# Optimization experiments

Measured on AMD Instinct MI355X. Metric: run time of the kernel, lower is better.

The kernel has to match this reference:

```python
import jax, jax.numpy as jnp
import numpy as np


def conv2d(x, w, b, pad=0, groups=1):
    y = jax.lax.conv_general_dilated(
        x, w, (1, 1), [(pad, pad), (pad, pad)],
        dimension_numbers=('NCHW', 'OIHW', 'NCHW'), feature_group_count=groups)
    return y + b[None, :, None, None]


def layernorm(x, w, b, eps=1e-5):
    # per-pixel LayerNorm over channel dim (matches to_3d -> nn.LayerNorm(dim) -> to_4d)
    mu = x.mean(1, keepdims=True)
    var = ((x - mu) ** 2).mean(1, keepdims=True)
    return (x - mu) * jax.lax.rsqrt(var + eps) * w[None, :, None, None] + b[None, :, None, None]


def setup_inputs():
    key = jax.random.key(0)
    ks = jax.random.split(key, 16)
    B, C, H, W = 1, 64, 64, 64
    heads, dh = 8, 8
    inner = heads * dh          # 64
    hid_lc = 32                 # max(16, inner // 2)
    hid_f = 4 * C               # 256, ffn_expansion_factor = 4
    def s(k, shape, fan):
        return (jax.random.normal(k, shape, jnp.float32) / np.float32(np.sqrt(fan)))
    return {
        'x': jax.random.normal(ks[0], (B, C, H, W), jnp.float32),
        'luma': jax.random.uniform(ks[1], (B, 1, H, W), jnp.float32),
        'ln1_w': jnp.ones((C,), jnp.float32), 'ln1_b': jnp.zeros((C,), jnp.float32),
        'qkv_w': s(ks[2], (3 * inner, C, 1, 1), C), 'qkv_b': jnp.zeros((3 * inner,), jnp.float32),
        'proj_w': s(ks[3], (C, inner, 1, 1), inner), 'proj_b': jnp.zeros((C,), jnp.float32),
        'lc1_w': s(ks[4], (hid_lc, 1, 3, 3), 9), 'lc1_b': jnp.zeros((hid_lc,), jnp.float32),
        'lc2_w': s(ks[5], (hid_lc, hid_lc, 3, 3), 9 * hid_lc), 'lc2_b': jnp.zeros((hid_lc,), jnp.float32),
        'gam_w': s(ks[6], (inner, hid_lc, 1, 1), hid_lc), 'gam_b': jnp.zeros((inner,), jnp.float32),
        'bet_w': s(ks[7], (inner, hid_lc, 1, 1), hid_lc), 'bet_b': jnp.zeros((inner,), jnp.float32),
        'alpha': jnp.float32(0.1),
        'ln2_w': jnp.ones((C,), jnp.float32), 'ln2_b': jnp.zeros((C,), jnp.float32),
        'ffn1_w': s(ks[8], (hid_f, C, 1, 1), C), 'ffn1_b': jnp.zeros((hid_f,), jnp.float32),
        'dw_w': s(ks[9], (hid_f, 1, 3, 3), 9), 'dw_b': jnp.zeros((hid_f,), jnp.float32),
        'ffn2_w': s(ks[10], (C, hid_f, 1, 1), hid_f), 'ffn2_b': jnp.zeros((C,), jnp.float32),
    }


def reference(x, luma, ln1_w, ln1_b, qkv_w, qkv_b, proj_w, proj_b,
              lc1_w, lc1_b, lc2_w, lc2_b, gam_w, gam_b, bet_w, bet_b, alpha,
              ln2_w, ln2_b, ffn1_w, ffn1_b, dw_w, dw_b, ffn2_w, ffn2_b):
    B, C, H, W = x.shape
    heads = 8
    N = H * W
    # --- attention branch ---
    xn = layernorm(x, ln1_w, ln1_b)
    qkv = conv2d(xn, qkv_w, qkv_b)             # [B, 3*inner, H, W]
    inner = qkv.shape[1] // 3
    dh = inner // heads

    def to_bhnd(t):  # b (h d) x y -> b h (x y) d
        return t.reshape(B, heads, dh, N).transpose(0, 1, 3, 2)

    q, k, v = [to_bhnd(t) for t in jnp.split(qkv, 3, axis=1)]
    # luma conditioning
    h1 = jax.nn.relu(conv2d(luma, lc1_w, lc1_b, pad=1))
    h1 = jax.nn.relu(conv2d(h1, lc2_w, lc2_b, pad=1))
    g = to_bhnd(conv2d(h1, gam_w, gam_b))
    bt = to_bhnd(conv2d(h1, bet_w, bet_b))
    q = g * q + bt
    k = g * k + bt
    v = g * v + bt
    # additive luma bias on q (avg_pool2d 3x3, count_include_pad=True -> fixed /9)
    invL = 1.0 - luma
    invL = jax.lax.reduce_window(invL, 0.0, jax.lax.add, (1, 1, 3, 3), (1, 1, 1, 1),
                                 [(0, 0), (0, 0), (1, 1), (1, 1)]) / 9.0
    invL = invL.reshape(B, N)
    invL = invL - invL.mean(-1, keepdims=True)
    q = q + alpha * invL[:, None, :, None]
    scale = dh ** -0.5
    attn = jax.nn.softmax(jnp.einsum('bhid,bhjd->bhij', q, k) * scale, axis=-1)
    out = jnp.einsum('bhij,bhjd->bhid', attn, v)
    out = out.transpose(0, 1, 3, 2).reshape(B, inner, H, W)
    x = x + conv2d(out, proj_w, proj_b)
    # --- ConvFFN branch ---
    y = layernorm(x, ln2_w, ln2_b)
    y = conv2d(y, ffn1_w, ffn1_b)
    y = conv2d(y, dw_w, dw_b, pad=1, groups=y.shape[1])
    y = jax.nn.gelu(y, approximate=False)
    y = conv2d(y, ffn2_w, ffn2_b)
    return x + y
```

## Files before the change

### kernel.cpp

```cpp
#include <hip/hip_runtime.h>
#include <math.h>

#define NPIX 4096
#define IMG 64
#define NBLK 512

typedef __attribute__((ext_vector_type(8))) short bf16x8;
typedef __attribute__((ext_vector_type(4))) float floatx4;
typedef __attribute__((ext_vector_type(4))) unsigned int uintx4;

__device__ __forceinline__ unsigned int split_pack(float x) {
  unsigned int u = __float_as_uint(x);
  unsigned int hif = u & 0xffff0000u;
  float lof = x - __uint_as_float(hif);
  return (u >> 16) | (__float_as_uint(lof) & 0xffff0000u);
}

__device__ __forceinline__ unsigned int pack_hi2(float a, float b) {
  return __builtin_amdgcn_perm(__float_as_uint(b), __float_as_uint(a),
                               0x07060302u);
}

__device__ __forceinline__ void stA_f32(float* p, float v) {
  __hip_atomic_store(p, v, __ATOMIC_RELAXED, __HIP_MEMORY_SCOPE_AGENT);
}
__device__ __forceinline__ void stA_u32(void* p, unsigned int v) {
  __hip_atomic_store((unsigned int*)p, v, __ATOMIC_RELAXED,
                     __HIP_MEMORY_SCOPE_AGENT);
}
__device__ __forceinline__ void stA_u64(void* p, unsigned long long v) {
  __hip_atomic_store((unsigned long long*)p, v, __ATOMIC_RELAXED,
                     __HIP_MEMORY_SCOPE_AGENT);
}
__device__ __forceinline__ unsigned int ldA(const unsigned int* p) {
  return __hip_atomic_load(p, __ATOMIC_RELAXED, __HIP_MEMORY_SCOPE_AGENT);
}
__device__ __forceinline__ unsigned int addA(unsigned int* p) {
  return __hip_atomic_fetch_add(p, 1u, __ATOMIC_RELAXED,
                                __HIP_MEMORY_SCOPE_AGENT);
}

__device__ __forceinline__ void gbar(unsigned int* base, int bid) {
  __syncthreads();
  if (threadIdx.x == 0) {
    int g = bid >> 6;
    unsigned int* ga = base + g * 32;
    unsigned int old = addA(ga);
    if (old == 63u) {
      addA(base + 256);
      while (ldA(base + 256) < 8u) __builtin_amdgcn_s_sleep(1);
      stA_u32(ga + 16, 1u);
    } else {
      while (ldA(ga + 16) == 0u) __builtin_amdgcn_s_sleep(2);
    }
    asm volatile("" ::: "memory");
  }
  __syncthreads();
}

struct S1 {
  float lum[144];
  float sw1[288];
  float tin[32][100];
  float swt[4][32][9];
  float red[64];
};
struct S2 {
  float xs[64][32];
  float wsh[64][64];
  float h2s[32][32];
  float wgs[32][64];
  float wbs[32][64];
  float mu[32];
  float rs[32];
};
struct S4 {
  float at[64][34];
  float wsh[64][64];
  float xsl[64][34];
  float ps[16][32];
  float pq[16][32];
  float mus[32];
  float rss[32];
};
struct S5 {
  float xs2[16][260];
  float wshT[32][260];
};
union SU {
  S1 s1;
  S2 s2;
  S4 s4;
  S5 s5;
};

__global__ void init_kernel(unsigned int* __restrict__ ctr,
                            unsigned short* __restrict__ cbuf) {
  int t = threadIdx.x;
#pragma unroll
  for (int i = 0; i < 8; i++) ctr[t + i * 256] = 0u;
  if (t < 16) cbuf[t] = (t < 8) ? 0x3F80 : 0;
}

__global__ __launch_bounds__(256, 3) void fused_kernel(
    const float* __restrict__ x, const float* __restrict__ luma,
    const float* __restrict__ lc1w, const float* __restrict__ lc1b,
    const float* __restrict__ lc2w, const float* __restrict__ lc2b,
    const float* __restrict__ ln1w, const float* __restrict__ ln1b,
    const float* __restrict__ qkvW, const float* __restrict__ qkvB,
    const float* __restrict__ gamW, const float* __restrict__ gamB,
    const float* __restrict__ betW, const float* __restrict__ betB,
    const float* __restrict__ alpha, const float* __restrict__ projW,
    const float* __restrict__ projB, const float* __restrict__ ln2w,
    const float* __restrict__ ln2b, const float* __restrict__ ffn1W,
    const float* __restrict__ ffn1B, const float* __restrict__ dww,
    const float* __restrict__ dwb, const float* __restrict__ ffn2W,
    const float* __restrict__ ffn2B, float* __restrict__ out,
    float* __restrict__ pooled, float* __restrict__ bsums,
    unsigned short* __restrict__ cbuf, float* __restrict__ mu1,
    float* __restrict__ rs1, unsigned short* __restrict__ qhl,
    unsigned short* __restrict__ khl, unsigned short* __restrict__ vthx,
    unsigned short* __restrict__ vtlx, float* __restrict__ pacc,
    float* __restrict__ pl, float* __restrict__ x1, float* __restrict__ f1,
    float* __restrict__ h2, unsigned int* __restrict__ ctr) {
  __shared__ SU u;
  int bid = blockIdx.x;
  int tid = threadIdx.x;

  {
    int tile = bid >> 3, ocg = bid & 7;
    int ty0 = (tile >> 3) * 8, tx0 = (tile & 7) * 8;
    float(&lum)[144] = u.s1.lum;
    float(&sw1)[288] = u.s1.sw1;
    float(&tin)[32][100] = u.s1.tin;
    float(&swt)[4][32][9] = u.s1.swt;
    float(&red)[64] = u.s1.red;
    if (tid < 144) {
      int py = tid / 12, px = tid - py * 12;
      int gy = ty0 + py - 2, gx = tx0 + px - 2;
      lum[tid] = (gy >= 0 && gy < IMG && gx >= 0 && gx < IMG)
                     ? luma[gy * IMG + gx]
                     : 0.f;
    }
    for (int idx = tid; idx < 288; idx += 256) sw1[idx] = lc1w[idx];
    for (int idx = tid; idx < 1152; idx += 256) {
      int o = idx / 288, r = idx - o * 288;
      swt[o][r / 9][r % 9] = lc2w[(ocg * 4 + o) * 288 + r];
    }
    __syncthreads();
    for (int idx = tid; idx < 3200; idx += 256) {
      int ic = idx / 100, pos = idx - ic * 100;
      int py = pos / 10, px = pos - py * 10;
      int gy = ty0 + py - 1, gx = tx0 + px - 1;
      float v = 0.f;
      if (gy >= 0 && gy < IMG && gx >= 0 && gx < IMG) {
        float s = lc1b[ic];
        const float* wp = &sw1[ic * 9];
#pragma unroll
        for (int dy = 0; dy < 3; dy++)
#pragma unroll
          for (int dx = 0; dx < 3; dx++)
            s = fmaf(wp[dy * 3 + dx], lum[(py + dy) * 12 + px + dx], s);
        v = fmaxf(s, 0.f);
      }
      tin[ic][pos] = v;
    }
    __syncthreads();
    int o = tid >> 6, pix = tid & 63;
    int ly = pix >> 3, lx = pix & 7;
    int p = (ty0 + ly) * IMG + tx0 + lx;
    float acc = lc2b[ocg * 4 + o];
    for (int ic = 0; ic < 32; ic++) {
      float v[9];
#pragma unroll
      for (int dy = 0; dy < 3; dy++)
#pragma unroll
        for (int dx = 0; dx < 3; dx++)
          v[dy * 3 + dx] = tin[ic][(ly + dy) * 10 + lx + dx];
#pragma unroll
      for (int t = 0; t < 9; t++) acc = fmaf(swt[o][ic][t], v[t], acc);
    }
    stA_f32(&h2[(ocg * 4 + o) * NPIX + p], fmaxf(acc, 0.f));
    if (ocg == 0) {
      if (tid < 64) {
        int gy = ty0 + ly, gx = tx0 + lx;
        float sv = 0.f;
#pragma unroll
        for (int dy = 0; dy < 3; dy++)
#pragma unroll
          for (int dx = 0; dx < 3; dx++)
            sv += lum[(ly + dy + 1) * 12 + lx + dx + 1];
        float cy = 3.f - (gy == 0 ? 1.f : 0.f) - (gy == 63 ? 1.f : 0.f);
        float cx = 3.f - (gx == 0 ? 1.f : 0.f) - (gx == 63 ? 1.f : 0.f);
        float pv = (cy * cx - sv) * (1.f / 9.f);
        stA_f32(&pooled[p], pv);
        red[tid] = pv;
      }
      __syncthreads();
      for (int st = 32; st > 0; st >>= 1) {
        if (tid < st) red[tid] += red[tid + st];
        __syncthreads();
      }
      if (tid == 0) stA_f32(&bsums[tile], red[0]);
      if (tid < 64) {
        float s = 0.f, q = 0.f;
#pragma unroll 8
        for (int cc = 0; cc < 64; cc++) {
          float xv = x[cc * NPIX + p];
          s += xv;
          q = fmaf(xv, xv, q);
        }
        float mu = s * (1.f / 64.f);
        stA_f32(&mu1[p], mu);
        stA_f32(&rs1[p], rsqrtf(q * (1.f / 64.f) - mu * mu + 1e-5f));
      }
    }
  }
  gbar(ctr + 0, bid);

  {
    const float QSCALE = 0.35355339059327376f * 1.4426950408889634f;
    float(&xs)[64][32] = u.s2.xs;
    float(&wsh)[64][64] = u.s2.wsh;
    float(&h2s)[32][32] = u.s2.h2s;
    float(&wgs)[32][64] = u.s2.wgs;
    float(&wbs)[32][64] = u.s2.wbs;
    float(&mu)[32] = u.s2.mu;
    float(&rs)[32] = u.s2.rs;
    int n0 = (bid & 127) * 32, part = bid >> 7;
    int m0 = (part < 2 ? part : 2) * 64;
    if (tid < 32) {
      mu[tid] = mu1[n0 + tid];
      rs[tid] = rs1[n0 + tid];
    }
    {
      int e = tid * 2;
      int c = e >> 3, off = (e & 7) * 4;
      *(float4*)&xs[c][off] = *(const float4*)&x[c * NPIX + n0 + off];
      int e1 = e + 1;
      int c1 = e1 >> 3, off1 = (e1 & 7) * 4;
      *(float4*)&xs[c1][off1] = *(const float4*)&x[c1 * NPIX + n0 + off1];
    }
    {
      int m = tid >> 2, kg = (tid & 3) * 16;
      const float4* wr = (const float4*)&qkvW[(m0 + m) * 64 + kg];
      float4 w0 = wr[0], w1 = wr[1], w2 = wr[2], w3 = wr[3];
      float wv[16] = {w0.x, w0.y, w0.z, w0.w, w1.x, w1.y, w1.z, w1.w,
                      w2.x, w2.y, w2.z, w2.w, w3.x, w3.y, w3.z, w3.w};
#pragma unroll
      for (int j = 0; j < 16; j++) wsh[kg + j][m] = wv[j];
    }
    {
      int k = tid >> 3, nf = (tid & 7) * 4;
      *(float4*)&h2s[k][nf] = *(const float4*)&h2[k * NPIX + n0 + nf];
    }
    {
      int m = tid >> 2, kg = (tid & 3) * 8;
      const float4* g0 = (const float4*)&gamW[m * 32 + kg];
      float4 a = g0[0], b4 = g0[1];
      float gv[8] = {a.x, a.y, a.z, a.w, b4.x, b4.y, b4.z, b4.w};
#pragma unroll
      for (int j = 0; j < 8; j++) wgs[kg + j][m] = gv[j];
      const float4* bb0 = (const float4*)&betW[m * 32 + kg];
      float4 c4 = bb0[0], d4 = bb0[1];
      float bv[8] = {c4.x, c4.y, c4.z, c4.w, d4.x, d4.y, d4.z, d4.w};
#pragma unroll
      for (int j = 0; j < 8; j++) wbs[kg + j][m] = bv[j];
    }
    __syncthreads();
    {
      int c = tid >> 2, pg = (tid & 3) * 8;
      float wc = ln1w[c], bc = ln1b[c];
#pragma unroll
      for (int j = 0; j < 8; j++) {
        int p = pg + j;
        xs[c][p] = (xs[c][p] - mu[p]) * rs[p] * wc + bc;
      }
    }
    __syncthreads();
    int tx = tid & 15, ty = tid >> 4;
    float ga[4][2] = {}, ba[4][2] = {};
#pragma unroll 8
    for (int kk = 0; kk < 32; kk++) {
      float4 wg4 = *(const float4*)&wgs[kk][ty * 4];
      float4 wb4 = *(const float4*)&wbs[kk][ty * 4];
      float2 h22 = *(const float2*)&h2s[kk][tx * 2];
      float gv[4] = {wg4.x, wg4.y, wg4.z, wg4.w};
      float bv[4] = {wb4.x, wb4.y, wb4.z, wb4.w};
      float hv[2] = {h22.x, h22.y};
#pragma unroll
      for (int im = 0; im < 4; im++)
#pragma unroll
        for (int in = 0; in < 2; in++) {
          ga[im][in] = fmaf(gv[im], hv[in], ga[im][in]);
          ba[im][in] = fmaf(bv[im], hv[in], ba[im][in]);
        }
    }
#pragma unroll
    for (int im = 0; im < 4; im++) {
      int cc = ty * 4 + im;
      float gb = gamB[cc], bb2 = betB[cc];
#pragma unroll
      for (int in = 0; in < 2; in++) {
        ga[im][in] += gb;
        ba[im][in] += bb2;
      }
    }
    float acc[4][2] = {};
#pragma unroll 8
    for (int kk = 0; kk < 64; kk++) {
      float4 a = *(const float4*)&wsh[kk][ty * 4];
      float2 b2 = *(const float2*)&xs[kk][tx * 2];
      float av[4] = {a.x, a.y, a.z, a.w};
      float bv[2] = {b2.x, b2.y};
#pragma unroll
      for (int im = 0; im < 4; im++)
#pragma unroll
        for (int in = 0; in < 2; in++)
          acc[im][in] = fmaf(av[im], bv[in], acc[im][in]);
    }
    float val[4][2];
#pragma unroll
    for (int im = 0; im < 4; im++) {
      int cc = ty * 4 + im;
      float bv = qkvB[m0 + cc];
#pragma unroll
      for (int in = 0; in < 2; in++)
        val[im][in] = fmaf(ga[im][in], acc[im][in] + bv, ba[im][in]);
    }
    if (part == 0) {
      float msum = 0.f;
      for (int t = 0; t < 64; t++) msum += bsums[t];
      float mean = msum * (1.f / 4096.f);
      float a0 = alpha[0];
      const float2 pv = *(const float2*)&pooled[n0 + tx * 2];
      float iv[2] = {a0 * (pv.x - mean), a0 * (pv.y - mean)};
#pragma unroll
      for (int im = 0; im < 4; im++)
#pragma unroll
        for (int in = 0; in < 2; in++)
          val[im][in] = (val[im][in] + iv[in]) * QSCALE;
    }
    if (part < 2) {
      unsigned short* dst = (part == 0) ? qhl : khl;
      int hh = ty >> 1, d0 = (ty & 1) * 4;
#pragma unroll
      for (int in = 0; in < 2; in++) {
        int n = n0 + tx * 2 + in;
        unsigned int pk[4];
#pragma unroll
        for (int im = 0; im < 4; im++) pk[im] = split_pack(val[im][in]);
        short4 hi, lo;
        hi.x = (short)(pk[0] & 0xffffu); hi.y = (short)(pk[1] & 0xffffu);
        hi.z = (short)(pk[2] & 0xffffu); hi.w = (short)(pk[3] & 0xffffu);
        lo.x = (short)(pk[0] >> 16); lo.y = (short)(pk[1] >> 16);
        lo.z = (short)(pk[2] >> 16); lo.w = (short)(pk[3] >> 16);
        unsigned short* base = dst + ((size_t)(hh * NPIX + n) << 4) + d0;
        stA_u64(base, __builtin_bit_cast(unsigned long long, hi));
        stA_u64(base + 8, __builtin_bit_cast(unsigned long long, lo));
      }
    } else {
      int nq = n0 + tx * 2;
      int off0 = (nq >> 5) * 32 + ((nq >> 4) & 1) * 4 + ((nq >> 2) & 3) * 8 +
                 (nq & 3);
#pragma unroll
      for (int im = 0; im < 4; im++) {
        int cc = ty * 4 + im;
        unsigned int pk0 = split_pack(val[im][0]);
        unsigned int pk1 = split_pack(val[im][1]);
        if (part == 2) {
          short2 hi;
          hi.x = (short)(pk0 & 0xffffu);
          hi.y = (short)(pk1 & 0xffffu);
          stA_u32(vthx + (size_t)cc * NPIX + off0,
                  __builtin_bit_cast(unsigned int, hi));
        } else {
          short2 lo;
          lo.x = (short)(pk0 >> 16);
          lo.y = (short)(pk1 >> 16);
          stA_u32(vtlx + (size_t)cc * NPIX + off0,
                  __builtin_bit_cast(unsigned int, lo));
        }
      }
    }
  }
  gbar(ctr + 512, bid);

  {
    int wave = tid >> 6, lane = tid & 63;
    int g = lane >> 4, c = lane & 15;
#pragma unroll 1
    for (int rep = 0; rep < 2; rep++) {
      int unit = bid * 2 + rep;
      int h = (unit >> 4) & 7, jp = unit >> 7;
      int i0 = (unit & 15) * 256 + wave * 64;
      int jbase = jp * 512;
      bf16x8 qB[4];
#pragma unroll
      for (int t = 0; t < 4; t++)
        qB[t] = *(const bf16x8*)(qhl +
                                 ((size_t)(h * NPIX + i0 + t * 16 + c) << 4) +
                                 ((g & 1) << 3));
      const unsigned short* kp =
          khl + ((size_t)(h * NPIX + jbase + c) << 4) + ((g >> 1) << 3);
      const unsigned short* vhp;
      const unsigned short* vlp;
      int vstep;
      if (c < 8) {
        vhp = vthx + (size_t)(h * 8 + c) * NPIX + jbase + (g << 3);
        vlp = vtlx + (size_t)(h * 8 + c) * NPIX + jbase + (g << 3);
        vstep = 32;
      } else {
        vhp = (c == 8) ? cbuf : (cbuf + 8);
        vlp = cbuf + 8;
        vstep = 0;
      }
      floatx4 zero4 = {0.f, 0.f, 0.f, 0.f};
      floatx4 aH[4], aM[4];
#pragma unroll
      for (int t = 0; t < 4; t++) {
        aH[t] = zero4;
        aM[t] = zero4;
      }
#pragma unroll 4
      for (int jt = 0; jt < 16; ++jt) {
        bf16x8 ka0 = *(const bf16x8*)kp;
        bf16x8 ka1 = *(const bf16x8*)(kp + 256);
        bf16x8 avh = *(const bf16x8*)vhp;
        bf16x8 avl = *(const bf16x8*)vlp;
        kp += 512;
        vhp += vstep;
        vlp += vstep;
#pragma unroll
        for (int t = 0; t < 4; t++) {
          floatx4 s0 = __builtin_amdgcn_mfma_f32_16x16x32_bf16(ka0, qB[t],
                                                               zero4, 0, 0, 0);
          floatx4 s1 = __builtin_amdgcn_mfma_f32_16x16x32_bf16(ka1, qB[t],
                                                               zero4, 0, 0, 0);
          float p0 = __builtin_amdgcn_exp2f(fminf(s0[0], 80.f));
          float p1 = __builtin_amdgcn_exp2f(fminf(s0[1], 80.f));
          float p2 = __builtin_amdgcn_exp2f(fminf(s0[2], 80.f));
          float p3 = __builtin_amdgcn_exp2f(fminf(s0[3], 80.f));
          float p4 = __builtin_amdgcn_exp2f(fminf(s1[0], 80.f));
          float p5 = __builtin_amdgcn_exp2f(fminf(s1[1], 80.f));
          float p6 = __builtin_amdgcn_exp2f(fminf(s1[2], 80.f));
          float p7 = __builtin_amdgcn_exp2f(fminf(s1[3], 80.f));
          uintx4 bh;
          bh.x = pack_hi2(p0, p1);
          bh.y = pack_hi2(p2, p3);
          bh.z = pack_hi2(p4, p5);
          bh.w = pack_hi2(p6, p7);
          bf16x8 pbh = __builtin_bit_cast(bf16x8, bh);
          aH[t] =
              __builtin_amdgcn_mfma_f32_16x16x32_bf16(avh, pbh, aH[t], 0, 0, 0);
          aM[t] =
              __builtin_amdgcn_mfma_f32_16x16x32_bf16(avl, pbh, aM[t], 0, 0, 0);
        }
      }
#pragma unroll
      for (int t = 0; t < 4; t++) {
        floatx4 o = aH[t] + aM[t];
        if (g < 2) {
          size_t b0 = (size_t)((jp * 8 + h) * NPIX + i0 + t * 16 + c);
          float2 lo2 = make_float2(o[0], o[1]);
          float2 hi2 = make_float2(o[2], o[3]);
          stA_u64(&pacc[b0 * 8 + g * 4],
                  __builtin_bit_cast(unsigned long long, lo2));
          stA_u64(&pacc[b0 * 8 + g * 4 + 2],
                  __builtin_bit_cast(unsigned long long, hi2));
        } else if (g == 2) {
          stA_f32(&pl[(size_t)((jp * 8 + h) * NPIX + i0 + t * 16 + c)], o[0]);
        }
      }
    }
  }
  gbar(ctr + 1024, bid);

  {
    float(&at)[64][34] = u.s4.at;
    float(&wsh)[64][64] = u.s4.wsh;
    float(&xsl)[64][34] = u.s4.xsl;
    float(&ps)[16][32] = u.s4.ps;
    float(&pq)[16][32] = u.s4.pq;
    float(&mus)[32] = u.s4.mus;
    float(&rss)[32] = u.s4.rss;
    int n0 = (bid & 127) * 32;
    int ch = bid >> 7;
    int mm = tid >> 2, kg = (tid & 3) * 16;
    {
      const float4* wr = (const float4*)&projW[mm * 64 + kg];
      float4 w0 = wr[0], w1 = wr[1], w2 = wr[2], w3 = wr[3];
      float wv[16] = {w0.x, w0.y, w0.z, w0.w, w1.x, w1.y, w1.z, w1.w,
                      w2.x, w2.y, w2.z, w2.w, w3.x, w3.y, w3.z, w3.w};
#pragma unroll
      for (int j = 0; j < 16; j++) wsh[kg + j][mm] = wv[j];
    }
    {
      int hh = tid >> 5, nn = tid & 31;
      int i = n0 + nn;
      float L = 0.f, o[8] = {};
#pragma unroll
      for (int p = 0; p < 8; p++) {
        size_t base = (size_t)((p * 8 + hh) * NPIX + i);
        L += pl[base];
        const float4 a0 = *(const float4*)&pacc[base * 8];
        const float4 a1 = *(const float4*)&pacc[base * 8 + 4];
        o[0] += a0.x; o[1] += a0.y; o[2] += a0.z; o[3] += a0.w;
        o[4] += a1.x; o[5] += a1.y; o[6] += a1.z; o[7] += a1.w;
      }
      float inv = 1.f / L;
#pragma unroll
      for (int d = 0; d < 8; d++) at[hh * 8 + d][nn] = o[d] * inv;
    }
    __syncthreads();
    int mq = tid >> 4, pp = (tid & 15) * 2;
    float acc[4][2] = {};
#pragma unroll 8
    for (int k = 0; k < 64; k++) {
      float4 w4 = *(const float4*)&wsh[k][mq * 4];
      float2 b2 = *(const float2*)&at[k][pp];
      acc[0][0] = fmaf(w4.x, b2.x, acc[0][0]);
      acc[0][1] = fmaf(w4.x, b2.y, acc[0][1]);
      acc[1][0] = fmaf(w4.y, b2.x, acc[1][0]);
      acc[1][1] = fmaf(w4.y, b2.y, acc[1][1]);
      acc[2][0] = fmaf(w4.z, b2.x, acc[2][0]);
      acc[2][1] = fmaf(w4.z, b2.y, acc[2][1]);
      acc[3][0] = fmaf(w4.w, b2.x, acc[3][0]);
      acc[3][1] = fmaf(w4.w, b2.y, acc[3][1]);
    }
    float v[4][2], sn0 = 0.f, sn1 = 0.f, qn0 = 0.f, qn1 = 0.f;
#pragma unroll
    for (int im = 0; im < 4; im++) {
      int row = mq * 4 + im;
      float bpv = projB[row];
      const float2 xr = *(const float2*)&x[row * NPIX + n0 + pp];
      float v0 = acc[im][0] + bpv + xr.x;
      float v1 = acc[im][1] + bpv + xr.y;
      v[im][0] = v0;
      v[im][1] = v1;
      sn0 += v0;
      qn0 = fmaf(v0, v0, qn0);
      sn1 += v1;
      qn1 = fmaf(v1, v1, qn1);
    }
    if (ch == 0) {
#pragma unroll
      for (int im = 0; im < 4; im++)
        stA_u64(&x1[(mq * 4 + im) * NPIX + n0 + pp],
                __builtin_bit_cast(unsigned long long,
                                   make_float2(v[im][0], v[im][1])));
    }
    ps[mq][pp] = sn0;
    ps[mq][pp + 1] = sn1;
    pq[mq][pp] = qn0;
    pq[mq][pp + 1] = qn1;
    __syncthreads();
    {
      const float4* w1r = (const float4*)&ffn1W[(ch * 64 + mm) * 64 + kg];
      float4 u0 = w1r[0], u1 = w1r[1], u2 = w1r[2], u3 = w1r[3];
      float uv[16] = {u0.x, u0.y, u0.z, u0.w, u1.x, u1.y, u1.z, u1.w,
                      u2.x, u2.y, u2.z, u2.w, u3.x, u3.y, u3.z, u3.w};
#pragma unroll
      for (int j = 0; j < 16; j++) wsh[kg + j][mm] = uv[j];
    }
    if (tid < 32) {
      float s = 0.f, q = 0.f;
#pragma unroll
      for (int t = 0; t < 16; t++) {
        s += ps[t][tid];
        q += pq[t][tid];
      }
      float mu = s * (1.f / 64.f);
      mus[tid] = mu;
      rss[tid] = rsqrtf(q * (1.f / 64.f) - mu * mu + 1e-5f);
    }
    __syncthreads();
    {
      float mu0 = mus[pp], mu1v = mus[pp + 1];
      float rs0 = rss[pp], rs1v = rss[pp + 1];
#pragma unroll
      for (int im = 0; im < 4; im++) {
        int row = mq * 4 + im;
        float w2v = ln2w[row], b2v = ln2b[row];
        *(float2*)&xsl[row][pp] =
            make_float2((v[im][0] - mu0) * rs0 * w2v + b2v,
                        (v[im][1] - mu1v) * rs1v * w2v + b2v);
      }
    }
    __syncthreads();
    float a2[4][2] = {};
#pragma unroll 8
    for (int k = 0; k < 64; k++) {
      float4 w4 = *(const float4*)&wsh[k][mq * 4];
      float2 b2 = *(const float2*)&xsl[k][pp];
      a2[0][0] = fmaf(w4.x, b2.x, a2[0][0]);
      a2[0][1] = fmaf(w4.x, b2.y, a2[0][1]);
      a2[1][0] = fmaf(w4.y, b2.x, a2[1][0]);
      a2[1][1] = fmaf(w4.y, b2.y, a2[1][1]);
      a2[2][0] = fmaf(w4.z, b2.x, a2[2][0]);
      a2[2][1] = fmaf(w4.z, b2.y, a2[2][1]);
      a2[3][0] = fmaf(w4.w, b2.x, a2[3][0]);
      a2[3][1] = fmaf(w4.w, b2.y, a2[3][1]);
    }
#pragma unroll
    for (int im = 0; im < 4; im++) {
      int row = ch * 64 + mq * 4 + im;
      float bb = ffn1B[row];
      stA_u64(&f1[row * NPIX + n0 + pp],
              __builtin_bit_cast(unsigned long long,
                                 make_float2(a2[im][0] + bb, a2[im][1] + bb)));
    }
  }
  gbar(ctr + 1536, bid);

  {
    float(&xs2)[16][260] = u.s5.xs2;
    float(&wshT)[32][260] = u.s5.wshT;
    int n0 = (bid & 255) * 16, m0 = (bid >> 8) * 32;
    int y = n0 >> 6, x0 = n0 & 63;
    {
      int mm = tid >> 3, kg = (tid & 7) * 32;
      const float4* src = (const float4*)&ffn2W[(m0 + mm) * 256 + kg];
      float4* dst = (float4*)&wshT[mm][kg];
#pragma unroll
      for (int i = 0; i < 8; i++) dst[i] = src[i];
    }
    {
      int px4 = (tid & 3) * 4;
      int xabs = x0 + px4;
#pragma unroll
      for (int k = 0; k < 4; k++) {
        int c = (tid >> 2) + 64 * k;
        const float* base = f1 + c * NPIX;
        float wv[9];
#pragma unroll
        for (int i = 0; i < 9; i++) wv[i] = dww[c * 9 + i];
        float bc = dwb[c];
        float a[4] = {bc, bc, bc, bc};
#pragma unroll
        for (int dy = 0; dy < 3; dy++) {
          int yy = y + dy - 1;
          if (yy < 0 || yy > 63) continue;
          const float* row = base + yy * IMG + xabs;
          float4 mid = *(const float4*)row;
          float left = (xabs > 0) ? row[-1] : 0.f;
          float right = (xabs + 4 < IMG) ? row[4] : 0.f;
          float win[6] = {left, mid.x, mid.y, mid.z, mid.w, right};
#pragma unroll
          for (int o = 0; o < 4; o++)
#pragma unroll
            for (int dx = 0; dx < 3; dx++)
              a[o] = fmaf(wv[dy * 3 + dx], win[o + dx], a[o]);
        }
#pragma unroll
        for (int o = 0; o < 4; o++)
          xs2[px4 + o][c] =
              0.5f * a[o] * (1.f + erff(a[o] * 0.70710678118654752f));
      }
    }
    __syncthreads();
    int m = tid >> 3, np = (tid & 7) * 2;
    float a0 = 0.f, a1 = 0.f;
#pragma unroll 4
    for (int k4 = 0; k4 < 64; k4++) {
      float4 w4 = *(const float4*)&wshT[m][k4 * 4];
      float4 xa = *(const float4*)&xs2[np][k4 * 4];
      float4 xb = *(const float4*)&xs2[np + 1][k4 * 4];
      a0 = fmaf(w4.x, xa.x, a0);
      a1 = fmaf(w4.x, xb.x, a1);
      a0 = fmaf(w4.y, xa.y, a0);
      a1 = fmaf(w4.y, xb.y, a1);
      a0 = fmaf(w4.z, xa.z, a0);
      a1 = fmaf(w4.z, xb.z, a1);
      a0 = fmaf(w4.w, xa.w, a0);
      a1 = fmaf(w4.w, xb.w, a1);
    }
    int row = m0 + m;
    float bv = ffn2B[row];
    const float2 rr = *(const float2*)&x1[row * NPIX + n0 + np];
    *(float2*)&out[row * NPIX + n0 + np] =
        make_float2(a0 + bv + rr.x, a1 + bv + rr.y);
  }
}

extern "C" void kernel_launch(void* const* d_in, const int* in_sizes, int n_in,
                              void* d_out, int out_size, void* d_ws,
                              size_t ws_size, hipStream_t stream) {
  const float* x      = (const float*)d_in[0];
  const float* luma   = (const float*)d_in[1];
  const float* ln1_w  = (const float*)d_in[2];
  const float* ln1_b  = (const float*)d_in[3];
  const float* qkv_w  = (const float*)d_in[4];
  const float* qkv_b  = (const float*)d_in[5];
  const float* proj_w = (const float*)d_in[6];
  const float* proj_b = (const float*)d_in[7];
  const float* lc1_w  = (const float*)d_in[8];
  const float* lc1_b  = (const float*)d_in[9];
  const float* lc2_w  = (const float*)d_in[10];
  const float* lc2_b  = (const float*)d_in[11];
  const float* gam_w  = (const float*)d_in[12];
  const float* gam_b  = (const float*)d_in[13];
  const float* bet_w  = (const float*)d_in[14];
  const float* bet_b  = (const float*)d_in[15];
  const float* alpha  = (const float*)d_in[16];
  const float* ln2_w  = (const float*)d_in[17];
  const float* ln2_b  = (const float*)d_in[18];
  const float* ffn1_w = (const float*)d_in[19];
  const float* ffn1_b = (const float*)d_in[20];
  const float* dw_w   = (const float*)d_in[21];
  const float* dw_b   = (const float*)d_in[22];
  const float* ffn2_w = (const float*)d_in[23];
  const float* ffn2_b = (const float*)d_in[24];
  float* out = (float*)d_out;

  float* w = (float*)d_ws;
  float* pooled = w + 0;
  float* bsums  = w + 4096;
  unsigned short* cbuf = (unsigned short*)(w + 4160);
  float* mu1 = w + 4224;
  float* rs1 = w + 8320;
  unsigned short* qhl  = (unsigned short*)(w + 12416);
  unsigned short* khl  = (unsigned short*)(w + 274560);
  unsigned short* vthx = (unsigned short*)(w + 536704);
  unsigned short* vtlx = (unsigned short*)(w + 667776);
  float* pacc = w + 798848;
  float* pl   = w + 2896000;
  float* x1   = w + 3158144;
  float* f1   = w + 3420288;
  float* h2   = w + 4468864;
  unsigned int* ctr = (unsigned int*)(w + 4599936);

  init_kernel<<<1, 256, 0, stream>>>(ctr, cbuf);
  fused_kernel<<<dim3(NBLK), 256, 0, stream>>>(
      x, luma, lc1_w, lc1_b, lc2_w, lc2_b, ln1_w, ln1_b, qkv_w, qkv_b, gam_w,
      gam_b, bet_w, bet_b, alpha, proj_w, proj_b, ln2_w, ln2_b, ffn1_w, ffn1_b,
      dw_w, dw_b, ffn2_w, ffn2_b, out, pooled, bsums, cbuf, mu1, rs1, qhl, khl,
      vthx, vtlx, pacc, pl, x1, f1, h2, ctr);
}
```

Before: 208.9 us.

## Recompute LN1 stats locally and halve attention key splits per block

LayerNorm-1 mean and rstd are now computed in stage 2 from the x tile already in shared memory, using a two-level reduction. This removes the phase-1 per-pixel pass over x and the global mu1/rs1 round trip. The attention stage also changes from two work units per block over 512 keys each to one unit per block over 1024 keys, so there are 4 key partitions instead of 8. The projection stage therefore sums 4 partial accumulators instead of 8. This cuts partial-sum traffic and reduction work, at the cost of a longer serial key loop per block and some redundant stats work across the three qkv parts.

```diff
diff --git a/kernel.cpp b/kernel.cpp
--- a/kernel.cpp
+++ b/kernel.cpp
@@ -71,6 +71,8 @@
   float h2s[32][32];
   float wgs[32][64];
   float wbs[32][64];
+  float pss[8][32];
+  float pqq[8][32];
   float mu[32];
   float rs[32];
 };
@@ -117,8 +119,7 @@
     const float* __restrict__ dwb, const float* __restrict__ ffn2W,
     const float* __restrict__ ffn2B, float* __restrict__ out,
     float* __restrict__ pooled, float* __restrict__ bsums,
-    unsigned short* __restrict__ cbuf, float* __restrict__ mu1,
-    float* __restrict__ rs1, unsigned short* __restrict__ qhl,
+    unsigned short* __restrict__ cbuf, unsigned short* __restrict__ qhl,
     unsigned short* __restrict__ khl, unsigned short* __restrict__ vthx,
     unsigned short* __restrict__ vtlx, float* __restrict__ pacc,
     float* __restrict__ pl, float* __restrict__ x1, float* __restrict__ f1,
@@ -202,18 +203,6 @@
         __syncthreads();
       }
       if (tid == 0) stA_f32(&bsums[tile], red[0]);
-      if (tid < 64) {
-        float s = 0.f, q = 0.f;
-#pragma unroll 8
-        for (int cc = 0; cc < 64; cc++) {
-          float xv = x[cc * NPIX + p];
-          s += xv;
-          q = fmaf(xv, xv, q);
-        }
-        float mu = s * (1.f / 64.f);
-        stA_f32(&mu1[p], mu);
-        stA_f32(&rs1[p], rsqrtf(q * (1.f / 64.f) - mu * mu + 1e-5f));
-      }
     }
   }
   gbar(ctr + 0, bid);
@@ -225,14 +214,12 @@
     float(&h2s)[32][32] = u.s2.h2s;
     float(&wgs)[32][64] = u.s2.wgs;
     float(&wbs)[32][64] = u.s2.wbs;
+    float(&pss)[8][32] = u.s2.pss;
+    float(&pqq)[8][32] = u.s2.pqq;
     float(&mu)[32] = u.s2.mu;
     float(&rs)[32] = u.s2.rs;
     int n0 = (bid & 127) * 32, part = bid >> 7;
     int m0 = (part < 2 ? part : 2) * 64;
-    if (tid < 32) {
-      mu[tid] = mu1[n0 + tid];
-      rs[tid] = rs1[n0 + tid];
-    }
     {
       int e = tid * 2;
       int c = e >> 3, off = (e & 7) * 4;
@@ -266,6 +253,31 @@
       float bv[8] = {c4.x, c4.y, c4.z, c4.w, d4.x, d4.y, d4.z, d4.w};
 #pragma unroll
       for (int j = 0; j < 8; j++) wbs[kg + j][m] = bv[j];
+    }
+    __syncthreads();
+    {
+      int p = tid & 31, i = tid >> 5;
+      float s = 0.f, q = 0.f;
+#pragma unroll
+      for (int j = 0; j < 8; j++) {
+        float xv = xs[i * 8 + j][p];
+        s += xv;
+        q = fmaf(xv, xv, q);
+      }
+      pss[i][p] = s;
+      pqq[i][p] = q;
+    }
+    __syncthreads();
+    if (tid < 32) {
+      float s = 0.f, q = 0.f;
+#pragma unroll
+      for (int i = 0; i < 8; i++) {
+        s += pss[i][tid];
+        q += pqq[i][tid];
+      }
+      float m = s * (1.f / 64.f);
+      mu[tid] = m;
+      rs[tid] = rsqrtf(q * (1.f / 64.f) - m * m + 1e-5f);
     }
     __syncthreads();
     {
@@ -389,88 +401,84 @@
   {
     int wave = tid >> 6, lane = tid & 63;
     int g = lane >> 4, c = lane & 15;
-#pragma unroll 1
-    for (int rep = 0; rep < 2; rep++) {
-      int unit = bid * 2 + rep;
-      int h = (unit >> 4) & 7, jp = unit >> 7;
-      int i0 = (unit & 15) * 256 + wave * 64;
-      int jbase = jp * 512;
-      bf16x8 qB[4];
-#pragma unroll
-      for (int t = 0; t < 4; t++)
-        qB[t] = *(const bf16x8*)(qhl +
-                                 ((size_t)(h * NPIX + i0 + t * 16 + c) << 4) +
-                                 ((g & 1) << 3));
-      const unsigned short* kp =
-          khl + ((size_t)(h * NPIX + jbase + c) << 4) + ((g >> 1) << 3);
-      const unsigned short* vhp;
-      const unsigned short* vlp;
-      int vstep;
-      if (c < 8) {
-        vhp = vthx + (size_t)(h * 8 + c) * NPIX + jbase + (g << 3);
-        vlp = vtlx + (size_t)(h * 8 + c) * NPIX + jbase + (g << 3);
-        vstep = 32;
-      } else {
-        vhp = (c == 8) ? cbuf : (cbuf + 8);
-        vlp = cbuf + 8;
-        vstep = 0;
-      }
-      floatx4 zero4 = {0.f, 0.f, 0.f, 0.f};
-      floatx4 aH[4], aM[4];
+    int h = (bid >> 4) & 7, jp = bid >> 7;
+    int i0 = (bid & 15) * 256 + wave * 64;
+    int jbase = jp * 1024;
+    bf16x8 qB[4];
+#pragma unroll
+    for (int t = 0; t < 4; t++)
+      qB[t] = *(const bf16x8*)(qhl +
+                               ((size_t)(h * NPIX + i0 + t * 16 + c) << 4) +
+                               ((g & 1) << 3));
+    const unsigned short* kp =
+        khl + ((size_t)(h * NPIX + jbase + c) << 4) + ((g >> 1) << 3);
+    const unsigned short* vhp;
+    const unsigned short* vlp;
+    int vstep;
+    if (c < 8) {
+      vhp = vthx + (size_t)(h * 8 + c) * NPIX + jbase + (g << 3);
+      vlp = vtlx + (size_t)(h * 8 + c) * NPIX + jbase + (g << 3);
+      vstep = 32;
+    } else {
+      vhp = (c == 8) ? cbuf : (cbuf + 8);
+      vlp = cbuf + 8;
+      vstep = 0;
+    }
+    floatx4 zero4 = {0.f, 0.f, 0.f, 0.f};
+    floatx4 aH[4], aM[4];
+#pragma unroll
+    for (int t = 0; t < 4; t++) {
+      aH[t] = zero4;
+      aM[t] = zero4;
+    }
+#pragma unroll 4
+    for (int jt = 0; jt < 32; ++jt) {
+      bf16x8 ka0 = *(const bf16x8*)kp;
+      bf16x8 ka1 = *(const bf16x8*)(kp + 256);
+      bf16x8 avh = *(const bf16x8*)vhp;
+      bf16x8 avl = *(const bf16x8*)vlp;
+      kp += 512;
+      vhp += vstep;
+      vlp += vstep;
 #pragma unroll
       for (int t = 0; t < 4; t++) {
-        aH[t] = zero4;
-        aM[t] = zero4;
-      }
-#pragma unroll 4
-      for (int jt = 0; jt < 16; ++jt) {
-        bf16x8 ka0 = *(const bf16x8*)kp;
-        bf16x8 ka1 = *(const bf16x8*)(kp + 256);
-        bf16x8 avh = *(const bf16x8*)vhp;
-        bf16x8 avl = *(const bf16x8*)vlp;
-        kp += 512;
-        vhp += vstep;
-        vlp += vstep;
-#pragma unroll
-        for (int t = 0; t < 4; t++) {
-          floatx4 s0 = __builtin_amdgcn_mfma_f32_16x16x32_bf16(ka0, qB[t],
-                                                               zero4, 0, 0, 0);
-          floatx4 s1 = __builtin_amdgcn_mfma_f32_16x16x32_bf16(ka1, qB[t],
-                                                               zero4, 0, 0, 0);
-          float p0 = __builtin_amdgcn_exp2f(fminf(s0[0], 80.f));
-          float p1 = __builtin_amdgcn_exp2f(fminf(s0[1], 80.f));
-          float p2 = __builtin_amdgcn_exp2f(fminf(s0[2], 80.f));
-          float p3 = __builtin_amdgcn_exp2f(fminf(s0[3], 80.f));
-          float p4 = __builtin_amdgcn_exp2f(fminf(s1[0], 80.f));
-          float p5 = __builtin_amdgcn_exp2f(fminf(s1[1], 80.f));
-          float p6 = __builtin_amdgcn_exp2f(fminf(s1[2], 80.f));
-          float p7 = __builtin_amdgcn_exp2f(fminf(s1[3], 80.f));
-          uintx4 bh;
-          bh.x = pack_hi2(p0, p1);
-          bh.y = pack_hi2(p2, p3);
-          bh.z = pack_hi2(p4, p5);
-          bh.w = pack_hi2(p6, p7);
-          bf16x8 pbh = __builtin_bit_cast(bf16x8, bh);
-          aH[t] =
-              __builtin_amdgcn_mfma_f32_16x16x32_bf16(avh, pbh, aH[t], 0, 0, 0);
-          aM[t] =
-              __builtin_amdgcn_mfma_f32_16x16x32_bf16(avl, pbh, aM[t], 0, 0, 0);
-        }
-      }
-#pragma unroll
-      for (int t = 0; t < 4; t++) {
-        floatx4 o = aH[t] + aM[t];
-        if (g < 2) {
-          size_t b0 = (size_t)((jp * 8 + h) * NPIX + i0 + t * 16 + c);
-          float2 lo2 = make_float2(o[0], o[1]);
-          float2 hi2 = make_float2(o[2], o[3]);
-          stA_u64(&pacc[b0 * 8 + g * 4],
-                  __builtin_bit_cast(unsigned long long, lo2));
-          stA_u64(&pacc[b0 * 8 + g * 4 + 2],
-                  __builtin_bit_cast(unsigned long long, hi2));
-        } else if (g == 2) {
-          stA_f32(&pl[(size_t)((jp * 8 + h) * NPIX + i0 + t * 16 + c)], o[0]);
-        }
+        floatx4 s0 = __builtin_amdgcn_mfma_f32_16x16x32_bf16(ka0, qB[t],
+                                                             zero4, 0, 0, 0);
+        floatx4 s1 = __builtin_amdgcn_mfma_f32_16x16x32_bf16(ka1, qB[t],
+                                                             zero4, 0, 0, 0);
+        float p0 = __builtin_amdgcn_exp2f(fminf(s0[0], 80.f));
+        float p1 = __builtin_amdgcn_exp2f(fminf(s0[1], 80.f));
+        float p2 = __builtin_amdgcn_exp2f(fminf(s0[2], 80.f));
+        float p3 = __builtin_amdgcn_exp2f(fminf(s0[3], 80.f));
+        float p4 = __builtin_amdgcn_exp2f(fminf(s1[0], 80.f));
+        float p5 = __builtin_amdgcn_exp2f(fminf(s1[1], 80.f));
+        float p6 = __builtin_amdgcn_exp2f(fminf(s1[2], 80.f));
+        float p7 = __builtin_amdgcn_exp2f(fminf(s1[3], 80.f));
+        uintx4 bh;
+        bh.x = pack_hi2(p0, p1);
+        bh.y = pack_hi2(p2, p3);
+        bh.z = pack_hi2(p4, p5);
+        bh.w = pack_hi2(p6, p7);
+        bf16x8 pbh = __builtin_bit_cast(bf16x8, bh);
+        aH[t] =
+            __builtin_amdgcn_mfma_f32_16x16x32_bf16(avh, pbh, aH[t], 0, 0, 0);
+        aM[t] =
+            __builtin_amdgcn_mfma_f32_16x16x32_bf16(avl, pbh, aM[t], 0, 0, 0);
+      }
+    }
+#pragma unroll
+    for (int t = 0; t < 4; t++) {
+      floatx4 o = aH[t] + aM[t];
+      if (g < 2) {
+        size_t b0 = (size_t)((jp * 8 + h) * NPIX + i0 + t * 16 + c);
+        float2 lo2 = make_float2(o[0], o[1]);
+        float2 hi2 = make_float2(o[2], o[3]);
+        stA_u64(&pacc[b0 * 8 + g * 4],
+                __builtin_bit_cast(unsigned long long, lo2));
+        stA_u64(&pacc[b0 * 8 + g * 4 + 2],
+                __builtin_bit_cast(unsigned long long, hi2));
+      } else if (g == 2) {
+        stA_f32(&pl[(size_t)((jp * 8 + h) * NPIX + i0 + t * 16 + c)], o[0]);
       }
     }
   }
@@ -500,7 +508,7 @@
       int i = n0 + nn;
       float L = 0.f, o[8] = {};
 #pragma unroll
-      for (int p = 0; p < 8; p++) {
+      for (int p = 0; p < 4; p++) {
         size_t base = (size_t)((p * 8 + hh) * NPIX + i);
         L += pl[base];
         const float4 a0 = *(const float4*)&pacc[base * 8];
@@ -717,8 +725,6 @@
   float* pooled = w + 0;
   float* bsums  = w + 4096;
   unsigned short* cbuf = (unsigned short*)(w + 4160);
-  float* mu1 = w + 4224;
-  float* rs1 = w + 8320;
   unsigned short* qhl  = (unsigned short*)(w + 12416);
   unsigned short* khl  = (unsigned short*)(w + 274560);
   unsigned short* vthx = (unsigned short*)(w + 536704);
@@ -734,6 +740,6 @@
   fused_kernel<<<dim3(NBLK), 256, 0, stream>>>(
       x, luma, lc1_w, lc1_b, lc2_w, lc2_b, ln1_w, ln1_b, qkv_w, qkv_b, gam_w,
       gam_b, bet_w, bet_b, alpha, proj_w, proj_b, ln2_w, ln2_b, ffn1_w, ffn1_b,
-      dw_w, dw_b, ffn2_w, ffn2_b, out, pooled, bsums, cbuf, mu1, rs1, qhl, khl,
+      dw_w, dw_b, ffn2_w, ffn2_b, out, pooled, bsums, cbuf, qhl, khl,
       vthx, vtlx, pacc, pl, x1, f1, h2, ctr);
 }
```

After: 202.0 us. 3.3% less time.
